# Kernel tuning notes

Measured on AMD Instinct MI355X. Metric: run time of the kernel, lower is better.

The kernel has to match this reference:

```python
import jax, jax.numpy as jnp
import numpy as np

NUM_HEADS = 12


def setup_inputs() -> dict:
    key = jax.random.key(0)
    ks = jax.random.split(key, 9)
    R, C, B, E = 128, 256, 1, 768
    s = 1.0 / np.sqrt(E)
    return {
        "x": jax.random.normal(ks[0], (R, C, B, E), jnp.float32),
        "wq": jax.random.normal(ks[1], (E, E), jnp.float32) * s,
        "bq": jax.random.normal(ks[2], (E,), jnp.float32) * 0.02,
        "wk": jax.random.normal(ks[3], (E, E), jnp.float32) * s,
        "bk": jax.random.normal(ks[4], (E,), jnp.float32) * 0.02,
        "wv": jax.random.normal(ks[5], (E, E), jnp.float32) * s,
        "bv": jax.random.normal(ks[6], (E,), jnp.float32) * 0.02,
        "wo": jax.random.normal(ks[7], (E, E), jnp.float32) * s,
        "bo": jax.random.normal(ks[8], (E,), jnp.float32) * 0.02,
    }


def reference(x, wq, bq, wk, bk, wv, bv, wo, bo):
    R, C, B, E = x.shape
    H = NUM_HEADS
    D = E // H
    # scaling = head_dim^-0.5 / sqrt(num_rows)  (tied row attention)
    scaling = (D ** -0.5) / jnp.sqrt(jnp.asarray(R, x.dtype))
    q = (x @ wq + bq).reshape(R, C, B, H, D) * scaling
    k = (x @ wk + bk).reshape(R, C, B, H, D)
    v = (x @ wv + bv).reshape(R, C, B, H, D)
    # tied attention: contract QK^T over rows as well as head_dim
    attn_weights = jnp.einsum('ribhd,rjbhd->hbij', q, k)
    attn_probs = jax.nn.softmax(attn_weights, axis=-1)
    # same probs reused for every row
    context = jnp.einsum('hbij,rjbhd->ribhd', attn_probs, v)
    context = context.reshape(R, C, B, E)
    output = context @ wo + bo
    return (output, attn_probs)
```

## Files before the change

kernel.cpp:

```cpp
#include <hip/hip_runtime.h>
#include <hip/hip_bf16.h>
#include <stdint.h>

typedef __attribute__((ext_vector_type(4))) float f32x4;
typedef __attribute__((ext_vector_type(8))) short bf16x8;

__device__ __forceinline__ unsigned short f2bf(float f) {
  union { float f; unsigned u; } v; v.f = f;
  unsigned r = v.u + 0x7fffu + ((v.u >> 16) & 1u);
  return (unsigned short)(r >> 16);
}

#define GLL16(g, l)                                                   \
  __builtin_amdgcn_global_load_lds(                                   \
      (__attribute__((address_space(1))) void*)(g),                   \
      (__attribute__((address_space(3))) void*)(l), 16, 0, 0)

__global__ __launch_bounds__(256) void k_conv_x(const float* __restrict__ x,
                                                unsigned short* __restrict__ xb) {
  int i = blockIdx.x * 256 + threadIdx.x;
  float4 v = ((const float4*)x)[i];
  ushort4 o;
  o.x = f2bf(v.x); o.y = f2bf(v.y); o.z = f2bf(v.z); o.w = f2bf(v.w);
  ((ushort4*)xb)[i] = o;
}

__global__ __launch_bounds__(256) void k_conv_wT(const float* __restrict__ wq,
                                                 const float* __restrict__ wk,
                                                 const float* __restrict__ wv,
                                                 const float* __restrict__ wo,
                                                 unsigned short* __restrict__ WT) {
  __shared__ unsigned short tile[32][33];
  int t = blockIdx.z;
  const float* w = (t == 0) ? wq : (t == 1) ? wk : (t == 2) ? wv : wo;
  int k0 = blockIdx.x * 32, n0 = blockIdx.y * 32;
  int tx = threadIdx.x, ty = threadIdx.y;
#pragma unroll
  for (int s = 0; s < 32; s += 8)
    tile[tx][ty + s] = f2bf(w[(size_t)(k0 + ty + s) * 768 + n0 + tx]);
  __syncthreads();
#pragma unroll
  for (int s = 0; s < 32; s += 8)
    WT[(size_t)t * 589824 + (size_t)(n0 + ty + s) * 768 + k0 + tx] = tile[ty + s][tx];
}

__device__ __forceinline__ void gemm256_core(const char* __restrict__ Ag,
                                             const char* __restrict__ Bg,
                                             char* lds, int tid,
                                             f32x4 (&acc)[8][4]) {
  const int lane = tid & 63, w = tid >> 6;
  const int wm = w >> 2, wn = w & 3;
  const int fr = lane & 15, kb = (lane >> 4) * 16;
  const bool stageB = (w >= 4);
  const char* Sg = stageB ? Bg : Ag;
  const int wrow0 = 64 * (w & 3);
  const int srow = lane >> 2;
  const int slotL = lane & 3;

#pragma unroll
  for (int t = 0; t < 3; ++t) {
    char* dslot = lds + t * 32768 + (stageB ? 16384 : 0);
#pragma unroll
    for (int c = 0; c < 4; ++c) {
      int row = wrow0 + c * 16 + srow;
      int sG = slotL ^ ((row >> 1) & 3);
      GLL16(Sg + (size_t)row * 1536 + t * 64 + sG * 16,
            dslot + (wrow0 + c * 16) * 64);
    }
  }

  for (int t = 0; t < 24; ++t) {
    if (t < 22)       asm volatile("s_waitcnt vmcnt(8)" ::: "memory");
    else if (t == 22) asm volatile("s_waitcnt vmcnt(4)" ::: "memory");
    else              asm volatile("s_waitcnt vmcnt(0)" ::: "memory");
    __builtin_amdgcn_s_barrier();

    const char* slot = lds + (t & 3) * 32768;
    bf16x8 af[8], bfr[4];
#pragma unroll
    for (int fm = 0; fm < 8; ++fm) {
      int row = wm * 128 + fm * 16 + fr;
      af[fm] = *(const bf16x8*)(slot + row * 64 + (kb ^ (((row >> 1) & 3) << 4)));
    }
#pragma unroll
    for (int fn = 0; fn < 4; ++fn) {
      int row = wn * 64 + fn * 16 + fr;
      bfr[fn] = *(const bf16x8*)(slot + 16384 + row * 64 + (kb ^ (((row >> 1) & 3) << 4)));
    }

    if (t + 3 < 24) {
      char* dslot = lds + ((t + 3) & 3) * 32768 + (stageB ? 16384 : 0);
#pragma unroll
      for (int c = 0; c < 4; ++c) {
        int row = wrow0 + c * 16 + srow;
        int sG = slotL ^ ((row >> 1) & 3);
        GLL16(Sg + (size_t)row * 1536 + (t + 3) * 64 + sG * 16,
              dslot + (wrow0 + c * 16) * 64);
      }
    }

    __builtin_amdgcn_s_setprio(1);
#pragma unroll
    for (int fm = 0; fm < 8; ++fm)
#pragma unroll
      for (int fn = 0; fn < 4; ++fn)
        acc[fm][fn] = __builtin_amdgcn_mfma_f32_16x16x32_bf16(af[fm], bfr[fn],
                                                              acc[fm][fn], 0, 0, 0);
    __builtin_amdgcn_s_setprio(0);
  }
}

__global__ __launch_bounds__(512, 1) void k_gemm_qkv(const unsigned short* __restrict__ Xb,
                                                     const unsigned short* __restrict__ WT,
                                                     const float* __restrict__ bq,
                                                     const float* __restrict__ bk_,
                                                     const float* __restrict__ bv,
                                                     unsigned short* __restrict__ Q,
                                                     unsigned short* __restrict__ K,
                                                     unsigned short* __restrict__ V,
                                                     float qscale) {
  __shared__ __align__(16) char lds[131072];
  const int tid = threadIdx.x, lane = tid & 63, w = tid >> 6;
  const int bid = blockIdx.x;
  const int swz = (bid & 7) * 144 + (bid >> 3);
  const int mt = swz / 9, nt = swz % 9;
  const int m0 = mt * 256;
  const int t = nt / 3, n0 = (nt % 3) * 256;

  const unsigned short* Wt = WT + (size_t)t * 589824;
  const float* bias = (t == 0) ? bq : (t == 1) ? bk_ : bv;
  unsigned short* Out = (t == 0) ? Q : (t == 1) ? K : V;
  const float scale = (t == 0) ? qscale : 1.0f;

  f32x4 acc[8][4];
#pragma unroll
  for (int a = 0; a < 8; ++a)
#pragma unroll
    for (int b = 0; b < 4; ++b) acc[a][b] = (f32x4){0.f, 0.f, 0.f, 0.f};

  gemm256_core((const char*)Xb + (size_t)m0 * 1536,
               (const char*)Wt + (size_t)n0 * 1536, lds, tid, acc);

  const int wm = w >> 2, wn = w & 3;
  const int fr = lane & 15, rowb = (lane >> 4) * 4;
#pragma unroll
  for (int fm = 0; fm < 8; ++fm)
#pragma unroll
    for (int fn = 0; fn < 4; ++fn) {
      int col = n0 + wn * 64 + fn * 16 + fr;
      float b = bias[col];
#pragma unroll
      for (int rg = 0; rg < 4; ++rg) {
        int row = m0 + wm * 128 + fm * 16 + rowb + rg;
        Out[(size_t)row * 768 + col] = f2bf((acc[fm][fn][rg] + b) * scale);
      }
    }
}

__global__ __launch_bounds__(512, 1) void k_gemm_out(const unsigned short* __restrict__ Cb,
                                                     const unsigned short* __restrict__ WTo,
                                                     const float* __restrict__ bo,
                                                     float* __restrict__ Outp) {
  __shared__ __align__(16) char lds[131072];
  const int tid = threadIdx.x, lane = tid & 63, w = tid >> 6;
  const int bid = blockIdx.x;
  const int swz = (bid & 7) * 48 + (bid >> 3);
  const int mt = swz / 3, nt = swz % 3;
  const int m0 = mt * 256, n0 = nt * 256;

  f32x4 acc[8][4];
#pragma unroll
  for (int a = 0; a < 8; ++a)
#pragma unroll
    for (int b = 0; b < 4; ++b) acc[a][b] = (f32x4){0.f, 0.f, 0.f, 0.f};

  gemm256_core((const char*)Cb + (size_t)m0 * 1536,
               (const char*)WTo + (size_t)n0 * 1536, lds, tid, acc);

  const int wm = w >> 2, wn = w & 3;
  const int fr = lane & 15, rowb = (lane >> 4) * 4;
#pragma unroll
  for (int fm = 0; fm < 8; ++fm)
#pragma unroll
    for (int fn = 0; fn < 4; ++fn) {
      int col = n0 + wn * 64 + fn * 16 + fr;
      float b = bo[col];
#pragma unroll
      for (int rg = 0; rg < 4; ++rg) {
        int row = m0 + wm * 128 + fm * 16 + rowb + rg;
        Outp[(size_t)row * 768 + col] = acc[fm][fn][rg] + b;
      }
    }
}

__global__ __launch_bounds__(256) void k_attn(const unsigned short* __restrict__ Q,
                                              const unsigned short* __restrict__ Kb,
                                              float* __restrict__ logits) {
  __shared__ __align__(16) unsigned short As[2][128 * 64];
  __shared__ __align__(16) unsigned short Bs[2][128 * 64];
  const int tid = threadIdx.x, lane = tid & 63, w = tid >> 6;
  const int bid = blockIdx.x;
  const int tile = bid & 3;
  const int h = (bid >> 2) % 12;
  const int rs = bid / 48;
  const int i0 = (tile >> 1) * 128, j0 = (tile & 1) * 128;
  const int wm = w >> 1, wn = w & 1;
  const int rl8 = lane >> 3, cb8 = (lane & 7) * 16;
  const int fr = lane & 15, kb = (lane >> 4) * 16;

  f32x4 acc[4][4];
#pragma unroll
  for (int a = 0; a < 4; ++a)
#pragma unroll
    for (int b = 0; b < 4; ++b) acc[a][b] = (f32x4){0.f, 0.f, 0.f, 0.f};

  auto stage = [&](int rr) {
    int r = rs * 16 + rr;
    int p = rr & 1;
#pragma unroll
    for (int c = 0; c < 4; ++c) {
      int row = w * 32 + c * 8 + rl8;
      GLL16((const char*)Q + (size_t)(r * 256 + i0 + row) * 1536 + h * 128 + cb8,
            (char*)As[p] + w * 4096 + c * 1024);
      GLL16((const char*)Kb + (size_t)(r * 256 + j0 + row) * 1536 + h * 128 + cb8,
            (char*)Bs[p] + w * 4096 + c * 1024);
    }
  };

  stage(0);
  for (int rr = 0; rr < 16; ++rr) {
    __syncthreads();
    if (rr + 1 < 16) stage(rr + 1);
    const int p = rr & 1;
#pragma unroll
    for (int kk = 0; kk < 2; ++kk) {
      bf16x8 af[4], bfr[4];
#pragma unroll
      for (int fm = 0; fm < 4; ++fm)
        af[fm] = *(const bf16x8*)((const char*)As[p] + (wm * 64 + fm * 16 + fr) * 128 + kk * 64 + kb);
#pragma unroll
      for (int fn = 0; fn < 4; ++fn)
        bfr[fn] = *(const bf16x8*)((const char*)Bs[p] + (wn * 64 + fn * 16 + fr) * 128 + kk * 64 + kb);
#pragma unroll
      for (int fm = 0; fm < 4; ++fm)
#pragma unroll
        for (int fn = 0; fn < 4; ++fn)
          acc[fm][fn] = __builtin_amdgcn_mfma_f32_16x16x32_bf16(af[fm], bfr[fn],
                                                                acc[fm][fn], 0, 0, 0);
    }
  }

  float* lg = logits + (size_t)h * 65536;
  const int rowb = (lane >> 4) * 4;
#pragma unroll
  for (int fm = 0; fm < 4; ++fm)
#pragma unroll
    for (int fn = 0; fn < 4; ++fn) {
      int jj = j0 + wn * 64 + fn * 16 + fr;
#pragma unroll
      for (int rg = 0; rg < 4; ++rg) {
        int ii = i0 + wm * 64 + fm * 16 + rowb + rg;
        atomicAdd(&lg[ii * 256 + jj], acc[fm][fn][rg]);
      }
    }
}

__global__ __launch_bounds__(256) void k_softmax(const float* __restrict__ lg,
                                                 float* __restrict__ pout,
                                                 unsigned short* __restrict__ pbf) {
  const int row = blockIdx.x;
  const int j = threadIdx.x;
  const int lane = j & 63, wv = j >> 6;
  float v = lg[(size_t)row * 256 + j];
  float m = v;
#pragma unroll
  for (int o = 32; o; o >>= 1) m = fmaxf(m, __shfl_xor(m, o, 64));
  __shared__ float sm[4], ss[4];
  if (lane == 0) sm[wv] = m;
  __syncthreads();
  m = fmaxf(fmaxf(sm[0], sm[1]), fmaxf(sm[2], sm[3]));
  float e = __expf(v - m);
  float s = e;
#pragma unroll
  for (int o = 32; o; o >>= 1) s += __shfl_xor(s, o, 64);
  if (lane == 0) ss[wv] = s;
  __syncthreads();
  s = ss[0] + ss[1] + ss[2] + ss[3];
  float p = e / s;
  pout[(size_t)row * 256 + j] = p;
  pbf[(size_t)row * 256 + j] = f2bf(p);
}

__global__ __launch_bounds__(256) void k_pv(const unsigned short* __restrict__ P,
                                            const unsigned short* __restrict__ V,
                                            unsigned short* __restrict__ Cb) {
  __shared__ __align__(16) unsigned short Ps[2][256 * 32];
  __shared__ __align__(16) unsigned short Vs[2][32 * 64];
  const int tid = threadIdx.x, lane = tid & 63, w = tid >> 6;
  const int bid = blockIdx.x;
  const int h = bid % 12, r = bid / 12;
  const int fr = lane & 15, kb = (lane >> 4) * 16;
  const int rl4 = lane >> 2, cb4 = (lane & 3) * 16;
  const int rl8 = lane >> 3, cb8 = (lane & 7) * 16;

  f32x4 acc[4][4];
#pragma unroll
  for (int a = 0; a < 4; ++a)
#pragma unroll
    for (int b = 0; b < 4; ++b) acc[a][b] = (f32x4){0.f, 0.f, 0.f, 0.f};

  const char* Ph = (const char*)P + (size_t)h * 131072;

  auto stage = [&](int jt) {
    int p = jt & 1;
#pragma unroll
    for (int c = 0; c < 4; ++c) {
      int row = w * 64 + c * 16 + rl4;
      GLL16(Ph + (size_t)row * 512 + jt * 64 + cb4,
            (char*)Ps[p] + w * 4096 + c * 1024);
    }
    {
      int row = w * 8 + rl8;
      GLL16((const char*)V + (size_t)(r * 256 + jt * 32 + row) * 1536 + h * 128 + cb8,
            (char*)Vs[p] + w * 1024);
    }
  };

  stage(0);
  for (int jt = 0; jt < 8; ++jt) {
    __syncthreads();
    if (jt + 1 < 8) stage(jt + 1);
    const int p = jt & 1;
    bf16x8 af[4];
#pragma unroll
    for (int fm = 0; fm < 4; ++fm)
      af[fm] = *(const bf16x8*)((const char*)Ps[p] + (w * 64 + fm * 16 + fr) * 64 + kb);
#pragma unroll
    for (int fn = 0; fn < 4; ++fn) {
      bf16x8 bvv;
#pragma unroll
      for (int e = 0; e < 8; ++e)
        bvv[e] = (short)Vs[p][(8 * (lane >> 4) + e) * 64 + fn * 16 + fr];
#pragma unroll
      for (int fm = 0; fm < 4; ++fm)
        acc[fm][fn] = __builtin_amdgcn_mfma_f32_16x16x32_bf16(af[fm], bvv,
                                                              acc[fm][fn], 0, 0, 0);
    }
  }

  const int rowb = (lane >> 4) * 4;
#pragma unroll
  for (int fm = 0; fm < 4; ++fm)
#pragma unroll
    for (int fn = 0; fn < 4; ++fn) {
      int col = h * 64 + fn * 16 + fr;
#pragma unroll
      for (int rg = 0; rg < 4; ++rg) {
        int m = r * 256 + w * 64 + fm * 16 + rowb + rg;
        Cb[(size_t)m * 768 + col] = f2bf(acc[fm][fn][rg]);
      }
    }
}

extern "C" void kernel_launch(void* const* d_in, const int* in_sizes, int n_in,
                              void* d_out, int out_size, void* d_ws, size_t ws_size,
                              hipStream_t stream) {
  const float* x  = (const float*)d_in[0];
  const float* wq = (const float*)d_in[1];
  const float* bq = (const float*)d_in[2];
  const float* wk = (const float*)d_in[3];
  const float* bk = (const float*)d_in[4];
  const float* wv = (const float*)d_in[5];
  const float* bv = (const float*)d_in[6];
  const float* wo = (const float*)d_in[7];
  const float* bo = (const float*)d_in[8];
  float* out = (float*)d_out;

  char* wsb = (char*)d_ws;
  unsigned short* Cb = (unsigned short*)(wsb + 0);
  unsigned short* Qb = (unsigned short*)(wsb + 50331648);
  unsigned short* Kb = (unsigned short*)(wsb + 100663296);
  unsigned short* Vb = (unsigned short*)(wsb + 150994944);
  unsigned short* WT = (unsigned short*)(wsb + 201326592);
  float*          Lg = (float*)(wsb + 206045184);
  unsigned short* Pb = (unsigned short*)(wsb + 209190912);

  const float qscale = 0.011048543456039806f;

  k_conv_x<<<24576, 256, 0, stream>>>(x, Cb);
  k_conv_wT<<<dim3(24, 24, 4), dim3(32, 8), 0, stream>>>(wq, wk, wv, wo, WT);
  k_gemm_qkv<<<1152, 512, 0, stream>>>(Cb, WT, bq, bk, bv, Qb, Kb, Vb, qscale);
  hipMemsetAsync(Lg, 0, (size_t)12 * 256 * 256 * 4, stream);
  k_attn<<<384, 256, 0, stream>>>(Qb, Kb, Lg);
  k_softmax<<<3072, 256, 0, stream>>>(Lg, out + 25165824, Pb);
  k_pv<<<1536, 256, 0, stream>>>(Pb, Vb, Cb);
  k_gemm_out<<<384, 512, 0, stream>>>(Cb, WT + (size_t)3 * 589824, bo, out);
}
```

Baseline: 288.9 us.

## Fuse fp32-to-bf16 conversion of x into the QKV GEMM A-tile load

Removes the standalone x conversion kernel and has the QKV GEMM load fp32 x tiles directly into LDS, converting to bf16 in registers with packed cvt instructions before the MFMAs. This avoids writing and re-reading a 48MB bf16 copy of x. In exchange, each GEMM block reads twice as many A bytes (fp32), and since every row tile is reused across 9 N-tiles, total A traffic from global/L2 grows. LDS use also grows and the pipeline is rewritten with a new staging layout.

```diff
diff --git a/kernel.cpp b/kernel.cpp
--- a/kernel.cpp
+++ b/kernel.cpp
@@ -11,19 +11,19 @@
   return (unsigned short)(r >> 16);
 }
 
+__device__ __forceinline__ bf16x8 cvt8(f32x4 lo, f32x4 hi) {
+  union { bf16x8 v; unsigned u[4]; } r;
+  asm("v_cvt_pk_bf16_f32 %0, %1, %2" : "=v"(r.u[0]) : "v"(lo[0]), "v"(lo[1]));
+  asm("v_cvt_pk_bf16_f32 %0, %1, %2" : "=v"(r.u[1]) : "v"(lo[2]), "v"(lo[3]));
+  asm("v_cvt_pk_bf16_f32 %0, %1, %2" : "=v"(r.u[2]) : "v"(hi[0]), "v"(hi[1]));
+  asm("v_cvt_pk_bf16_f32 %0, %1, %2" : "=v"(r.u[3]) : "v"(hi[2]), "v"(hi[3]));
+  return r.v;
+}
+
 #define GLL16(g, l)                                                   \
   __builtin_amdgcn_global_load_lds(                                   \
       (__attribute__((address_space(1))) void*)(g),                   \
       (__attribute__((address_space(3))) void*)(l), 16, 0, 0)
-
-__global__ __launch_bounds__(256) void k_conv_x(const float* __restrict__ x,
-                                                unsigned short* __restrict__ xb) {
-  int i = blockIdx.x * 256 + threadIdx.x;
-  float4 v = ((const float4*)x)[i];
-  ushort4 o;
-  o.x = f2bf(v.x); o.y = f2bf(v.y); o.z = f2bf(v.z); o.w = f2bf(v.w);
-  ((ushort4*)xb)[i] = o;
-}
 
 __global__ __launch_bounds__(256) void k_conv_wT(const float* __restrict__ wq,
                                                  const float* __restrict__ wk,
@@ -42,6 +42,69 @@
 #pragma unroll
   for (int s = 0; s < 32; s += 8)
     WT[(size_t)t * 589824 + (size_t)(n0 + ty + s) * 768 + k0 + tx] = tile[ty + s][tx];
+}
+
+__device__ __forceinline__ void gemm256x_core(const char* __restrict__ Ag,
+                                              const char* __restrict__ Bg,
+                                              char* lds, int tid,
+                                              f32x4 (&acc)[8][4]) {
+  const int lane = tid & 63, w = tid >> 6;
+  const int wm = w >> 2, wn = w & 3;
+  const int fr = lane & 15, kb16 = (lane >> 4) * 16;
+  const int c0 = (lane >> 4) * 2;
+  const int brow_sub = lane >> 2, bslot = lane & 3;
+
+  auto stage = [&](int t) {
+    char* base = lds + (t % 3) * 49152;
+    const char* As = Ag + (size_t)t * 128 + w * 16;
+#pragma unroll
+    for (int i = 0; i < 4; ++i)
+      GLL16(As + (size_t)(i * 64 + lane) * 3072, base + (w * 4 + i) * 1024);
+    const char* Bs = Bg + (size_t)t * 64;
+    char* bdst = base + 32768;
+#pragma unroll
+    for (int jj = 0; jj < 2; ++jj) {
+      int j = w * 2 + jj;
+      int row = j * 16 + brow_sub;
+      int sG = bslot ^ ((row >> 1) & 3);
+      GLL16(Bs + (size_t)row * 1536 + sG * 16, bdst + j * 1024);
+    }
+  };
+
+  stage(0); stage(1);
+
+  for (int t = 0; t < 24; ++t) {
+    if (t < 23) asm volatile("s_waitcnt vmcnt(6)" ::: "memory");
+    else        asm volatile("s_waitcnt vmcnt(0)" ::: "memory");
+    __builtin_amdgcn_s_barrier();
+
+    if (t + 2 < 24) stage(t + 2);
+
+    const char* base = lds + (t % 3) * 49152;
+    bf16x8 af[8], bfr[4];
+#pragma unroll
+    for (int fm = 0; fm < 8; ++fm) {
+      int rho = wm * 128 + fm * 16 + fr;
+      f32x4 lo = *(const f32x4*)(base + c0 * 4096 + rho * 16);
+      f32x4 hi = *(const f32x4*)(base + (c0 + 1) * 4096 + rho * 16);
+      af[fm] = cvt8(lo, hi);
+    }
+    const char* slotB = base + 32768;
+#pragma unroll
+    for (int fn = 0; fn < 4; ++fn) {
+      int row = wn * 64 + fn * 16 + fr;
+      bfr[fn] = *(const bf16x8*)(slotB + row * 64 + (kb16 ^ (((row >> 1) & 3) << 4)));
+    }
+
+    __builtin_amdgcn_s_setprio(1);
+#pragma unroll
+    for (int fm = 0; fm < 8; ++fm)
+#pragma unroll
+      for (int fn = 0; fn < 4; ++fn)
+        acc[fm][fn] = __builtin_amdgcn_mfma_f32_16x16x32_bf16(af[fm], bfr[fn],
+                                                              acc[fm][fn], 0, 0, 0);
+    __builtin_amdgcn_s_setprio(0);
+  }
 }
 
 __device__ __forceinline__ void gemm256_core(const char* __restrict__ Ag,
@@ -110,7 +173,7 @@
   }
 }
 
-__global__ __launch_bounds__(512, 1) void k_gemm_qkv(const unsigned short* __restrict__ Xb,
+__global__ __launch_bounds__(512, 1) void k_gemm_qkv(const float* __restrict__ X,
                                                      const unsigned short* __restrict__ WT,
                                                      const float* __restrict__ bq,
                                                      const float* __restrict__ bk_,
@@ -119,7 +182,7 @@
                                                      unsigned short* __restrict__ K,
                                                      unsigned short* __restrict__ V,
                                                      float qscale) {
-  __shared__ __align__(16) char lds[131072];
+  __shared__ __align__(16) char lds[147456];
   const int tid = threadIdx.x, lane = tid & 63, w = tid >> 6;
   const int bid = blockIdx.x;
   const int swz = (bid & 7) * 144 + (bid >> 3);
@@ -138,8 +201,8 @@
 #pragma unroll
     for (int b = 0; b < 4; ++b) acc[a][b] = (f32x4){0.f, 0.f, 0.f, 0.f};
 
-  gemm256_core((const char*)Xb + (size_t)m0 * 1536,
-               (const char*)Wt + (size_t)n0 * 1536, lds, tid, acc);
+  gemm256x_core((const char*)X + (size_t)m0 * 3072,
+                (const char*)Wt + (size_t)n0 * 1536, lds, tid, acc);
 
   const int wm = w >> 2, wn = w & 3;
   const int fr = lane & 15, rowb = (lane >> 4) * 4;
@@ -387,9 +450,8 @@
 
   const float qscale = 0.011048543456039806f;
 
-  k_conv_x<<<24576, 256, 0, stream>>>(x, Cb);
   k_conv_wT<<<dim3(24, 24, 4), dim3(32, 8), 0, stream>>>(wq, wk, wv, wo, WT);
-  k_gemm_qkv<<<1152, 512, 0, stream>>>(Cb, WT, bq, bk, bv, Qb, Kb, Vb, qscale);
+  k_gemm_qkv<<<1152, 512, 0, stream>>>(x, WT, bq, bk, bv, Qb, Kb, Vb, qscale);
   hipMemsetAsync(Lg, 0, (size_t)12 * 256 * 256 * 4, stream);
   k_attn<<<384, 256, 0, stream>>>(Qb, Kb, Lg);
   k_softmax<<<3072, 256, 0, stream>>>(Lg, out + 25165824, Pb);
```

Result: slower. 411.7 us (+42.5%).
